# Kernel tuning notes

Measured on AMD Instinct MI355X. Metric: run time of the kernel, lower is better.

## Reference

```python
import jax, jax.numpy as jnp
import numpy as np

VOCAB, EMB_DIM = 50000, 300
HIDDEN, OUT_DIM, N_ASPECTS = 256, 3, 8
BATCH, SEQ = 8192, 128


def setup_inputs() -> dict:
    key = jax.random.key(0)
    k1, k2, k3, k4, k5, k6, k7 = jax.random.split(key, 7)
    input_ids = jax.random.randint(k1, (BATCH, SEQ), 0, VOCAB, dtype=jnp.int64 if jax.config.jax_enable_x64 else jnp.int32)
    aspect_id = jax.random.randint(k2, (BATCH,), 0, N_ASPECTS, dtype=jnp.int32)
    emb = jax.random.normal(k3, (VOCAB, EMB_DIM), dtype=jnp.float32)
    # Per-aspect 2-layer MLP params, stacked along aspect axis. PyTorch Linear
    # init scale ~ U(-1/sqrt(fan_in), 1/sqrt(fan_in)).
    s1 = 1.0 / np.sqrt(EMB_DIM)
    s2 = 1.0 / np.sqrt(HIDDEN)
    W1 = jax.random.uniform(k4, (N_ASPECTS, EMB_DIM, HIDDEN), jnp.float32, -s1, s1)
    b1 = jax.random.uniform(k5, (N_ASPECTS, HIDDEN), jnp.float32, -s1, s1)
    W2 = jax.random.uniform(k6, (N_ASPECTS, HIDDEN, OUT_DIM), jnp.float32, -s2, s2)
    b2 = jax.random.uniform(k7, (N_ASPECTS, OUT_DIM), jnp.float32, -s2, s2)
    return {"input_ids": input_ids, "aspect_id": aspect_id, "emb": emb,
            "W1": W1, "b1": b1, "W2": W2, "b2": b2}


def reference(input_ids, aspect_id, emb, W1, b1, W2, b2):
    # Embedding lookup + mean-pool over sequence -> [B, EMB_DIM]
    x = emb[input_ids].mean(axis=1)
    # Run every sample through every aspect MLP (A is tiny: 8), then select.
    # Same math as per-sample routed MLP, but as A batched GEMMs.
    h = jax.nn.relu(jnp.einsum('bd,adh->abh', x, W1) + b1[:, None, :])  # [A,B,H]
    o = jnp.einsum('abh,aho->abo', h, W2) + b2[:, None, :]              # [A,B,O]
    # Select per-sample expert output: [B, OUT_DIM]
    o_b = jnp.transpose(o, (1, 0, 2))  # [B, A, O]
    return jnp.take_along_axis(o_b, aspect_id[:, None, None], axis=1)[:, 0, :]
```

## Files before the change

### kernel.cpp

```cpp
#include <hip/hip_runtime.h>

constexpr int EMB_DIM   = 300;
constexpr int HIDDEN    = 256;
constexpr int OUT_DIM   = 3;
constexpr int SEQ       = 128;
constexpr int N_ASPECTS = 8;
constexpr int TILE      = 32;
constexpr int MTILE     = 8;

__device__ __forceinline__ unsigned int bfbits(float f) {
  unsigned int u = __float_as_uint(f);
  return (u + 0x7fffu + ((u >> 16) & 1u)) >> 16;
}
__device__ __forceinline__ unsigned int pack2(float lo, float hi) {
  return bfbits(lo) | (bfbits(hi) << 16);
}
__device__ __forceinline__ float blo(unsigned int u) { return __uint_as_float(u << 16); }
__device__ __forceinline__ float bhi(unsigned int u) { return __uint_as_float(u & 0xffff0000u); }

__global__ __launch_bounds__(1024) void prep_kernel(
    const float* __restrict__ emb, unsigned int* __restrict__ emb16, int n8,
    const float* __restrict__ W1, unsigned int* __restrict__ w16, int nw8,
    const int* __restrict__ aspect, int B, int* __restrict__ perm, int nperm) {
  const int t = threadIdx.x;

  if (blockIdx.x != 0) {
    int i = (blockIdx.x - 1) * 1024 + t;
    const int stride = (gridDim.x - 1) * 1024;
    const int total8 = n8 + nw8;
    for (; i < total8; i += stride) {
      const float4* p;
      unsigned int* dst;
      int k;
      if (i < n8) { p = (const float4*)emb + (size_t)i * 2;        dst = emb16; k = i; }
      else        { p = (const float4*)W1  + (size_t)(i - n8) * 2; dst = w16;   k = i - n8; }
      float4 a = p[0], b = p[1];
      uint4 o;
      o.x = pack2(a.x, a.y); o.y = pack2(a.z, a.w);
      o.z = pack2(b.x, b.y); o.w = pack2(b.z, b.w);
      ((uint4*)dst)[k] = o;
    }
    return;
  }

  const int lane = t & 63, wave = t >> 6;
  __shared__ int wcnt[16][N_ASPECTS];
  __shared__ int cur[16][N_ASPECTS];

  for (int i = t; i < nperm; i += 1024) perm[i] = -1;

  int my_a[8];
  int cnt[N_ASPECTS];
#pragma unroll
  for (int q = 0; q < N_ASPECTS; ++q) cnt[q] = 0;
#pragma unroll
  for (int k = 0; k < 8; ++k) {
    int s = t + k * 1024;
    int a = (s < B) ? aspect[s] : -1;
    my_a[k] = a;
#pragma unroll
    for (int q = 0; q < N_ASPECTS; ++q) cnt[q] += (a == q);
  }
#pragma unroll
  for (int q = 0; q < N_ASPECTS; ++q) {
    int c = cnt[q];
    for (int off = 32; off > 0; off >>= 1) c += __shfl_down(c, off);
    if (lane == 0) wcnt[wave][q] = c;
  }
  __syncthreads();
  if (t == 0) {
    int base = 0;
    for (int q = 0; q < N_ASPECTS; ++q) {
      int tot = 0;
      for (int w = 0; w < 16; ++w) { cur[w][q] = base + tot; tot += wcnt[w][q]; }
      base += ((tot + TILE - 1) / TILE) * TILE;
    }
  }
  __syncthreads();

#pragma unroll
  for (int k = 0; k < 8; ++k) {
    int a = my_a[k];
    int s = t + k * 1024;
#pragma unroll
    for (int q = 0; q < N_ASPECTS; ++q) {
      unsigned long long m = __ballot(a == q);
      if (a == q) {
        int rank = __popcll(m & ((1ull << lane) - 1ull));
        int pos = cur[wave][q] + rank;
        perm[pos] = s;
        if (rank == __popcll(m) - 1) cur[wave][q] = pos + 1;
      }
    }
  }
}

__global__ __launch_bounds__(256) void pool_kernel(
    const int* __restrict__ ids, const unsigned short* __restrict__ emb16,
    float* __restrict__ x, int B) {
  const int wave = threadIdx.x >> 6, lane = threadIdx.x & 63;
  const int b = blockIdx.x * 4 + wave;
  if (b >= B) return;

  int r0 = ids[(size_t)b * SEQ + lane];
  int r1 = ids[(size_t)b * SEQ + lane + 64];

#pragma unroll
  for (int k = 2; k <= 128; k <<= 1) {
#pragma unroll
    for (int j = k >> 1; j >= 1; j >>= 1) {
      if (j == 64) {
        int lo = min(r0, r1), hi = max(r0, r1);
        r0 = lo; r1 = hi;
      } else {
        const bool up0 = ((lane & k) == 0);
        const bool up1 = (((lane + 64) & k) == 0);
        const bool side = ((lane & j) == 0);
        int o0 = __shfl_xor(r0, j);
        int o1 = __shfl_xor(r1, j);
        r0 = (side == up0) ? min(r0, o0) : max(r0, o0);
        r1 = (side == up1) ? min(r1, o1) : max(r1, o1);
      }
    }
  }

  __shared__ int sid[4][SEQ];
  sid[wave][lane]      = r0;
  sid[wave][lane + 64] = r1;
  __syncthreads();

  float a0 = 0.f, a1 = 0.f, a2 = 0.f, a3 = 0.f;
  float c0 = 0.f, c1 = 0.f, c2 = 0.f, c3 = 0.f;
#pragma unroll 4
  for (int s = 0; s < SEQ; ++s) {
    const uint2* __restrict__ r =
        (const uint2*)(emb16 + (size_t)sid[wave][s] * EMB_DIM);
    uint2 v = r[lane];
    a0 += blo(v.x); a1 += bhi(v.x); a2 += blo(v.y); a3 += bhi(v.y);
    if (lane < 11) {
      uint2 w = r[64 + lane];
      c0 += blo(w.x); c1 += bhi(w.x); c2 += blo(w.y); c3 += bhi(w.y);
    }
  }
  const float sc = 1.0f / (float)SEQ;
  float4* __restrict__ xr = (float4*)(x + (size_t)b * EMB_DIM);
  xr[lane] = make_float4(a0 * sc, a1 * sc, a2 * sc, a3 * sc);
  if (lane < 11)
    xr[64 + lane] = make_float4(c0 * sc, c1 * sc, c2 * sc, c3 * sc);
}

__global__ __launch_bounds__(256) void mlp_kernel(
    const float* __restrict__ x, const int* __restrict__ aspect,
    const int* __restrict__ perm,
    const unsigned short* __restrict__ w16, const float* __restrict__ b1,
    const float* __restrict__ W2, const float* __restrict__ b2,
    float* __restrict__ out) {
  const int t = threadIdx.x;
  const int wave = t >> 6, lane = t & 63;
  const int g = wave >> 1;
  const int kw = wave & 1;
  const int start = blockIdx.x * MTILE;

  __shared__ int ss[MTILE];
  __shared__ float xch[2][4][64][4];

  if (t < MTILE) ss[t] = perm[start + t];
  __syncthreads();
  const int s0 = ss[0];
  if (s0 < 0) return;
  const int a = aspect[s0];

  int smp[4];
  const float* xrow[4];
#pragma unroll
  for (int s = 0; s < 4; ++s) {
    int m = __builtin_amdgcn_readfirstlane(ss[g * 4 + s]);
    smp[s] = m;
    xrow[s] = x + (size_t)(m < 0 ? s0 : m) * EMB_DIM;
  }

  const unsigned short* __restrict__ w1r =
      w16 + (size_t)a * EMB_DIM * HIDDEN + 4 * lane;
  float4 acc[4];
  if (kw == 0) {
    const float4 bb = ((const float4*)(b1 + a * HIDDEN))[lane];
#pragma unroll
    for (int s = 0; s < 4; ++s) acc[s] = bb;
  } else {
#pragma unroll
    for (int s = 0; s < 4; ++s) acc[s] = make_float4(0.f, 0.f, 0.f, 0.f);
  }
  const int d0 = kw ? 160 : 0;
  const int d1 = kw ? EMB_DIM : 160;
#pragma unroll 2
  for (int d = d0; d < d1; d += 4) {
    float4 xv[4];
#pragma unroll
    for (int s = 0; s < 4; ++s) xv[s] = *(const float4*)(xrow[s] + d);
#pragma unroll
    for (int dd = 0; dd < 4; ++dd) {
      const uint2 wv = *(const uint2*)(w1r + (size_t)(d + dd) * HIDDEN);
      const float w0 = blo(wv.x), w1v = bhi(wv.x);
      const float w2v = blo(wv.y), w3v = bhi(wv.y);
#pragma unroll
      for (int s = 0; s < 4; ++s) {
        const float xs = dd == 0 ? xv[s].x : dd == 1 ? xv[s].y
                        : dd == 2 ? xv[s].z : xv[s].w;
        acc[s].x = fmaf(xs, w0,  acc[s].x);
        acc[s].y = fmaf(xs, w1v, acc[s].y);
        acc[s].z = fmaf(xs, w2v, acc[s].z);
        acc[s].w = fmaf(xs, w3v, acc[s].w);
      }
    }
  }

  if (kw == 0) {
    *(float4*)&xch[g][2][lane][0] = acc[2];
    *(float4*)&xch[g][3][lane][0] = acc[3];
  } else {
    *(float4*)&xch[g][0][lane][0] = acc[0];
    *(float4*)&xch[g][1][lane][0] = acc[1];
  }
  __syncthreads();

  const float4* __restrict__ w2p =
      (const float4*)(W2 + (size_t)a * HIDDEN * OUT_DIM + lane * 12);
  const float4 w2a = w2p[0];
  const float4 w2b = w2p[1];
  const float4 w2c = w2p[2];

  float4 own[2];
  int ms[2];
  if (kw == 0) {
    own[0] = acc[0]; own[1] = acc[1];
    ms[0] = smp[0];  ms[1] = smp[1];
  } else {
    own[0] = acc[2]; own[1] = acc[3];
    ms[0] = smp[2];  ms[1] = smp[3];
  }
  const int mys = 2 * kw;

  float p[2][OUT_DIM];
#pragma unroll
  for (int i = 0; i < 2; ++i) {
    const float4 pr = *(const float4*)&xch[g][mys + i][lane][0];
    const float h0 = fmaxf(own[i].x + pr.x, 0.f);
    const float h1 = fmaxf(own[i].y + pr.y, 0.f);
    const float h2 = fmaxf(own[i].z + pr.z, 0.f);
    const float h3 = fmaxf(own[i].w + pr.w, 0.f);
    p[i][0] = fmaf(h0, w2a.x, fmaf(h1, w2a.w, fmaf(h2, w2b.z, h3 * w2c.y)));
    p[i][1] = fmaf(h0, w2a.y, fmaf(h1, w2b.x, fmaf(h2, w2b.w, h3 * w2c.z)));
    p[i][2] = fmaf(h0, w2a.z, fmaf(h1, w2b.y, fmaf(h2, w2c.x, h3 * w2c.w)));
  }
#pragma unroll
  for (int off = 32; off > 0; off >>= 1)
#pragma unroll
    for (int i = 0; i < 2; ++i) {
      p[i][0] += __shfl_down(p[i][0], off);
      p[i][1] += __shfl_down(p[i][1], off);
      p[i][2] += __shfl_down(p[i][2], off);
    }

  if (lane == 0) {
    const float g0 = b2[a * OUT_DIM + 0];
    const float g1 = b2[a * OUT_DIM + 1];
    const float g2 = b2[a * OUT_DIM + 2];
#pragma unroll
    for (int i = 0; i < 2; ++i) {
      if (ms[i] >= 0) {
        float* o = out + (size_t)ms[i] * OUT_DIM;
        o[0] = p[i][0] + g0;
        o[1] = p[i][1] + g1;
        o[2] = p[i][2] + g2;
      }
    }
  }
}

extern "C" void kernel_launch(void* const* d_in, const int* in_sizes, int n_in,
                              void* d_out, int out_size, void* d_ws, size_t ws_size,
                              hipStream_t stream) {
  const int*   ids    = (const int*)d_in[0];
  const int*   aspect = (const int*)d_in[1];
  const float* emb    = (const float*)d_in[2];
  const float* W1     = (const float*)d_in[3];
  const float* b1     = (const float*)d_in[4];
  const float* W2     = (const float*)d_in[5];
  const float* b2     = (const float*)d_in[6];
  float*       out    = (float*)d_out;

  const int B     = in_sizes[1];
  const int nemb  = in_sizes[2];
  const int nw1   = in_sizes[3];
  const int nblk  = (B + TILE - 1) / TILE + N_ASPECTS;
  const int nperm = nblk * TILE;

  float* x    = (float*)d_ws;
  int*   perm = (int*)((char*)d_ws + (size_t)B * EMB_DIM * sizeof(float));
  unsigned short* emb16 =
      (unsigned short*)((char*)perm + (((size_t)nperm * 4 + 15) & ~(size_t)15));
  unsigned short* w16 = emb16 + (size_t)nemb;

  prep_kernel<<<513, 1024, 0, stream>>>(emb, (unsigned int*)emb16, nemb / 8,
                                        W1, (unsigned int*)w16, nw1 / 8,
                                        aspect, B, perm, nperm);
  pool_kernel<<<(B + 3) / 4, 256, 0, stream>>>(ids, emb16, x, B);
  mlp_kernel<<<nperm / MTILE, 256, 0, stream>>>(x, aspect, perm, w16, b1, W2, b2, out);
}
```

Measured before the change: 129.4 us.

## Fuse embedding mean-pool into aspect-sorted MLP kernel via shared memory

Merges the pooling kernel into the MLP kernel. Each block pools its 8 aspect-sorted samples, two per wave, and keeps the pooled vectors in shared memory instead of writing x to global memory and reading it back. This removes a kernel launch and the global round trip of the pooled activations. The cost is more shared memory per block and more registers per wave. Padded perm slots now repeat pooling for sample s0, and the pooling grid follows perm order rather than batch order.

After: 120.2 us (median of 2 runs). 7.1% less time.

```diff
diff --git a/kernel.cpp b/kernel.cpp
--- a/kernel.cpp
+++ b/kernel.cpp
@@ -95,89 +95,107 @@
   }
 }
 
-__global__ __launch_bounds__(256) void pool_kernel(
+__global__ __launch_bounds__(256) void fused_kernel(
     const int* __restrict__ ids, const unsigned short* __restrict__ emb16,
-    float* __restrict__ x, int B) {
-  const int wave = threadIdx.x >> 6, lane = threadIdx.x & 63;
-  const int b = blockIdx.x * 4 + wave;
-  if (b >= B) return;
-
-  int r0 = ids[(size_t)b * SEQ + lane];
-  int r1 = ids[(size_t)b * SEQ + lane + 64];
+    const int* __restrict__ aspect, const int* __restrict__ perm,
+    const unsigned short* __restrict__ w16, const float* __restrict__ b1,
+    const float* __restrict__ W2, const float* __restrict__ b2,
+    float* __restrict__ out) {
+  const int t = threadIdx.x;
+  const int wave = t >> 6, lane = t & 63;
+  const int start = blockIdx.x * MTILE;
+
+  __shared__ int   ss[MTILE];
+  __shared__ int   sid[MTILE][SEQ];
+  __shared__ float xs[MTILE][EMB_DIM + 4];
+  __shared__ float xch[2][4][64][4];
+
+  if (t < MTILE) ss[t] = perm[start + t];
+  __syncthreads();
+  const int s0 = ss[0];
+  if (s0 < 0) return;
+  const int a = aspect[s0];
+
+  const int sa = 2 * wave, sb = 2 * wave + 1;
+  const int ma = __builtin_amdgcn_readfirstlane(ss[sa] < 0 ? s0 : ss[sa]);
+  const int mb = __builtin_amdgcn_readfirstlane(ss[sb] < 0 ? s0 : ss[sb]);
+
+  int r0 = ids[(size_t)ma * SEQ + lane];
+  int r1 = ids[(size_t)ma * SEQ + lane + 64];
+  int r2 = ids[(size_t)mb * SEQ + lane];
+  int r3 = ids[(size_t)mb * SEQ + lane + 64];
 
 #pragma unroll
   for (int k = 2; k <= 128; k <<= 1) {
 #pragma unroll
     for (int j = k >> 1; j >= 1; j >>= 1) {
       if (j == 64) {
-        int lo = min(r0, r1), hi = max(r0, r1);
-        r0 = lo; r1 = hi;
+        int lo0 = min(r0, r1), hi0 = max(r0, r1);
+        int lo1 = min(r2, r3), hi1 = max(r2, r3);
+        r0 = lo0; r1 = hi0; r2 = lo1; r3 = hi1;
       } else {
         const bool up0 = ((lane & k) == 0);
         const bool up1 = (((lane + 64) & k) == 0);
         const bool side = ((lane & j) == 0);
         int o0 = __shfl_xor(r0, j);
         int o1 = __shfl_xor(r1, j);
+        int o2 = __shfl_xor(r2, j);
+        int o3 = __shfl_xor(r3, j);
         r0 = (side == up0) ? min(r0, o0) : max(r0, o0);
         r1 = (side == up1) ? min(r1, o1) : max(r1, o1);
+        r2 = (side == up0) ? min(r2, o2) : max(r2, o2);
+        r3 = (side == up1) ? min(r3, o3) : max(r3, o3);
       }
     }
   }
 
-  __shared__ int sid[4][SEQ];
-  sid[wave][lane]      = r0;
-  sid[wave][lane + 64] = r1;
-  __syncthreads();
-
-  float a0 = 0.f, a1 = 0.f, a2 = 0.f, a3 = 0.f;
-  float c0 = 0.f, c1 = 0.f, c2 = 0.f, c3 = 0.f;
+  sid[sa][lane]      = r0;
+  sid[sa][lane + 64] = r1;
+  sid[sb][lane]      = r2;
+  sid[sb][lane + 64] = r3;
+
+  float p0 = 0.f, p1 = 0.f, p2 = 0.f, p3 = 0.f;
+  float q0 = 0.f, q1 = 0.f, q2 = 0.f, q3 = 0.f;
+  float ta0 = 0.f, ta1 = 0.f, ta2 = 0.f, ta3 = 0.f;
+  float tb0 = 0.f, tb1 = 0.f, tb2 = 0.f, tb3 = 0.f;
+  const bool tail = (lane < 11);
+
 #pragma unroll 4
   for (int s = 0; s < SEQ; ++s) {
-    const uint2* __restrict__ r =
-        (const uint2*)(emb16 + (size_t)sid[wave][s] * EMB_DIM);
-    uint2 v = r[lane];
-    a0 += blo(v.x); a1 += bhi(v.x); a2 += blo(v.y); a3 += bhi(v.y);
-    if (lane < 11) {
-      uint2 w = r[64 + lane];
-      c0 += blo(w.x); c1 += bhi(w.x); c2 += blo(w.y); c3 += bhi(w.y);
-    }
-  }
+    const uint2* __restrict__ ra =
+        (const uint2*)(emb16 + (size_t)sid[sa][s] * EMB_DIM);
+    const uint2* __restrict__ rb =
+        (const uint2*)(emb16 + (size_t)sid[sb][s] * EMB_DIM);
+    uint2 va = ra[lane];
+    uint2 vb = rb[lane];
+    p0 += blo(va.x); p1 += bhi(va.x); p2 += blo(va.y); p3 += bhi(va.y);
+    q0 += blo(vb.x); q1 += bhi(vb.x); q2 += blo(vb.y); q3 += bhi(vb.y);
+    if (tail) {
+      uint2 wa = ra[64 + lane];
+      uint2 wb = rb[64 + lane];
+      ta0 += blo(wa.x); ta1 += bhi(wa.x); ta2 += blo(wa.y); ta3 += bhi(wa.y);
+      tb0 += blo(wb.x); tb1 += bhi(wb.x); tb2 += blo(wb.y); tb3 += bhi(wb.y);
+    }
+  }
+
   const float sc = 1.0f / (float)SEQ;
-  float4* __restrict__ xr = (float4*)(x + (size_t)b * EMB_DIM);
-  xr[lane] = make_float4(a0 * sc, a1 * sc, a2 * sc, a3 * sc);
-  if (lane < 11)
-    xr[64 + lane] = make_float4(c0 * sc, c1 * sc, c2 * sc, c3 * sc);
-}
-
-__global__ __launch_bounds__(256) void mlp_kernel(
-    const float* __restrict__ x, const int* __restrict__ aspect,
-    const int* __restrict__ perm,
-    const unsigned short* __restrict__ w16, const float* __restrict__ b1,
-    const float* __restrict__ W2, const float* __restrict__ b2,
-    float* __restrict__ out) {
-  const int t = threadIdx.x;
-  const int wave = t >> 6, lane = t & 63;
+  *(float4*)&xs[sa][4 * lane] = make_float4(p0 * sc, p1 * sc, p2 * sc, p3 * sc);
+  *(float4*)&xs[sb][4 * lane] = make_float4(q0 * sc, q1 * sc, q2 * sc, q3 * sc);
+  if (tail) {
+    *(float4*)&xs[sa][256 + 4 * lane] =
+        make_float4(ta0 * sc, ta1 * sc, ta2 * sc, ta3 * sc);
+    *(float4*)&xs[sb][256 + 4 * lane] =
+        make_float4(tb0 * sc, tb1 * sc, tb2 * sc, tb3 * sc);
+  }
+  __syncthreads();
+
   const int g = wave >> 1;
   const int kw = wave & 1;
-  const int start = blockIdx.x * MTILE;
-
-  __shared__ int ss[MTILE];
-  __shared__ float xch[2][4][64][4];
-
-  if (t < MTILE) ss[t] = perm[start + t];
-  __syncthreads();
-  const int s0 = ss[0];
-  if (s0 < 0) return;
-  const int a = aspect[s0];
 
   int smp[4];
-  const float* xrow[4];
-#pragma unroll
-  for (int s = 0; s < 4; ++s) {
-    int m = __builtin_amdgcn_readfirstlane(ss[g * 4 + s]);
-    smp[s] = m;
-    xrow[s] = x + (size_t)(m < 0 ? s0 : m) * EMB_DIM;
-  }
+#pragma unroll
+  for (int s = 0; s < 4; ++s)
+    smp[s] = __builtin_amdgcn_readfirstlane(ss[g * 4 + s]);
 
   const unsigned short* __restrict__ w1r =
       w16 + (size_t)a * EMB_DIM * HIDDEN + 4 * lane;
@@ -196,7 +214,7 @@
   for (int d = d0; d < d1; d += 4) {
     float4 xv[4];
 #pragma unroll
-    for (int s = 0; s < 4; ++s) xv[s] = *(const float4*)(xrow[s] + d);
+    for (int s = 0; s < 4; ++s) xv[s] = *(const float4*)&xs[g * 4 + s][d];
 #pragma unroll
     for (int dd = 0; dd < 4; ++dd) {
       const uint2 wv = *(const uint2*)(w1r + (size_t)(d + dd) * HIDDEN);
@@ -204,12 +222,12 @@
       const float w2v = blo(wv.y), w3v = bhi(wv.y);
 #pragma unroll
       for (int s = 0; s < 4; ++s) {
-        const float xs = dd == 0 ? xv[s].x : dd == 1 ? xv[s].y
-                        : dd == 2 ? xv[s].z : xv[s].w;
-        acc[s].x = fmaf(xs, w0,  acc[s].x);
-        acc[s].y = fmaf(xs, w1v, acc[s].y);
-        acc[s].z = fmaf(xs, w2v, acc[s].z);
-        acc[s].w = fmaf(xs, w3v, acc[s].w);
+        const float xsc = dd == 0 ? xv[s].x : dd == 1 ? xv[s].y
+                         : dd == 2 ? xv[s].z : xv[s].w;
+        acc[s].x = fmaf(xsc, w0,  acc[s].x);
+        acc[s].y = fmaf(xsc, w1v, acc[s].y);
+        acc[s].z = fmaf(xsc, w2v, acc[s].z);
+        acc[s].w = fmaf(xsc, w3v, acc[s].w);
       }
     }
   }
@@ -240,7 +258,7 @@
   }
   const int mys = 2 * kw;
 
-  float p[2][OUT_DIM];
+  float pp[2][OUT_DIM];
 #pragma unroll
   for (int i = 0; i < 2; ++i) {
     const float4 pr = *(const float4*)&xch[g][mys + i][lane][0];
@@ -248,17 +266,17 @@
     const float h1 = fmaxf(own[i].y + pr.y, 0.f);
     const float h2 = fmaxf(own[i].z + pr.z, 0.f);
     const float h3 = fmaxf(own[i].w + pr.w, 0.f);
-    p[i][0] = fmaf(h0, w2a.x, fmaf(h1, w2a.w, fmaf(h2, w2b.z, h3 * w2c.y)));
-    p[i][1] = fmaf(h0, w2a.y, fmaf(h1, w2b.x, fmaf(h2, w2b.w, h3 * w2c.z)));
-    p[i][2] = fmaf(h0, w2a.z, fmaf(h1, w2b.y, fmaf(h2, w2c.x, h3 * w2c.w)));
+    pp[i][0] = fmaf(h0, w2a.x, fmaf(h1, w2a.w, fmaf(h2, w2b.z, h3 * w2c.y)));
+    pp[i][1] = fmaf(h0, w2a.y, fmaf(h1, w2b.x, fmaf(h2, w2b.w, h3 * w2c.z)));
+    pp[i][2] = fmaf(h0, w2a.z, fmaf(h1, w2b.y, fmaf(h2, w2c.x, h3 * w2c.w)));
   }
 #pragma unroll
   for (int off = 32; off > 0; off >>= 1)
 #pragma unroll
     for (int i = 0; i < 2; ++i) {
-      p[i][0] += __shfl_down(p[i][0], off);
-      p[i][1] += __shfl_down(p[i][1], off);
-      p[i][2] += __shfl_down(p[i][2], off);
+      pp[i][0] += __shfl_down(pp[i][0], off);
+      pp[i][1] += __shfl_down(pp[i][1], off);
+      pp[i][2] += __shfl_down(pp[i][2], off);
     }
 
   if (lane == 0) {
@@ -269,9 +287,9 @@
     for (int i = 0; i < 2; ++i) {
       if (ms[i] >= 0) {
         float* o = out + (size_t)ms[i] * OUT_DIM;
-        o[0] = p[i][0] + g0;
-        o[1] = p[i][1] + g1;
-        o[2] = p[i][2] + g2;
+        o[0] = pp[i][0] + g0;
+        o[1] = pp[i][1] + g1;
+        o[2] = pp[i][2] + g2;
       }
     }
   }
@@ -295,8 +313,7 @@
   const int nblk  = (B + TILE - 1) / TILE + N_ASPECTS;
   const int nperm = nblk * TILE;
 
-  float* x    = (float*)d_ws;
-  int*   perm = (int*)((char*)d_ws + (size_t)B * EMB_DIM * sizeof(float));
+  int* perm = (int*)d_ws;
   unsigned short* emb16 =
       (unsigned short*)((char*)perm + (((size_t)nperm * 4 + 15) & ~(size_t)15));
   unsigned short* w16 = emb16 + (size_t)nemb;
@@ -304,6 +321,6 @@
   prep_kernel<<<513, 1024, 0, stream>>>(emb, (unsigned int*)emb16, nemb / 8,
                                         W1, (unsigned int*)w16, nw1 / 8,
                                         aspect, B, perm, nperm);
-  pool_kernel<<<(B + 3) / 4, 256, 0, stream>>>(ids, emb16, x, B);
-  mlp_kernel<<<nperm / MTILE, 256, 0, stream>>>(x, aspect, perm, w16, b1, W2, b2, out);
-}
+  fused_kernel<<<nperm / MTILE, 256, 0, stream>>>(ids, emb16, aspect, perm,
+                                                  w16, b1, W2, b2, out);
+}
```

## Fuse embedding pooling and aspect MLP into one kernel via shared memory

Applied to the files above, without the earlier changes.

Merges the pooling and MLP kernels into a single 512-thread kernel. Each wave pools one aspect-sorted sample into shared memory, then pairs of waves compute the MLP for two samples each. This removes the pooled x round trip through global memory and one launch. In exchange, the W1 reads are amortised over 2 samples per wave instead of 4, so weight traffic from cache doubles. Pooling also now runs over padded perm slots, which duplicate sample s0.

Result: slower. 164.0 us (+26.8%).

```diff
diff --git a/kernel.cpp b/kernel.cpp
--- a/kernel.cpp
+++ b/kernel.cpp
@@ -95,15 +95,31 @@
   }
 }
 
-__global__ __launch_bounds__(256) void pool_kernel(
+__global__ __launch_bounds__(512) void fused_kernel(
     const int* __restrict__ ids, const unsigned short* __restrict__ emb16,
-    float* __restrict__ x, int B) {
-  const int wave = threadIdx.x >> 6, lane = threadIdx.x & 63;
-  const int b = blockIdx.x * 4 + wave;
-  if (b >= B) return;
-
-  int r0 = ids[(size_t)b * SEQ + lane];
-  int r1 = ids[(size_t)b * SEQ + lane + 64];
+    const int* __restrict__ aspect, const int* __restrict__ perm,
+    const unsigned short* __restrict__ w16, const float* __restrict__ b1,
+    const float* __restrict__ W2, const float* __restrict__ b2,
+    float* __restrict__ out) {
+  const int t = threadIdx.x;
+  const int wave = t >> 6, lane = t & 63;
+  const int start = blockIdx.x * MTILE;
+
+  __shared__ int   ss[MTILE];
+  __shared__ int   sid[MTILE][SEQ];
+  __shared__ float xs[MTILE][EMB_DIM + 4];
+  __shared__ float xch[4][2][64][4];
+
+  if (t < MTILE) ss[t] = perm[start + t];
+  __syncthreads();
+  const int s0 = ss[0];
+  if (s0 < 0) return;
+  const int a = aspect[s0];
+
+  const int m = __builtin_amdgcn_readfirstlane(ss[wave] < 0 ? s0 : ss[wave]);
+
+  int r0 = ids[(size_t)m * SEQ + lane];
+  int r1 = ids[(size_t)m * SEQ + lane + 64];
 
 #pragma unroll
   for (int k = 2; k <= 128; k <<= 1) {
@@ -124,102 +140,72 @@
     }
   }
 
-  __shared__ int sid[4][SEQ];
   sid[wave][lane]      = r0;
   sid[wave][lane + 64] = r1;
-  __syncthreads();
 
   float a0 = 0.f, a1 = 0.f, a2 = 0.f, a3 = 0.f;
   float c0 = 0.f, c1 = 0.f, c2 = 0.f, c3 = 0.f;
+  const bool tail = (lane < 11);
 #pragma unroll 4
   for (int s = 0; s < SEQ; ++s) {
     const uint2* __restrict__ r =
         (const uint2*)(emb16 + (size_t)sid[wave][s] * EMB_DIM);
     uint2 v = r[lane];
     a0 += blo(v.x); a1 += bhi(v.x); a2 += blo(v.y); a3 += bhi(v.y);
-    if (lane < 11) {
+    if (tail) {
       uint2 w = r[64 + lane];
       c0 += blo(w.x); c1 += bhi(w.x); c2 += blo(w.y); c3 += bhi(w.y);
     }
   }
+
   const float sc = 1.0f / (float)SEQ;
-  float4* __restrict__ xr = (float4*)(x + (size_t)b * EMB_DIM);
-  xr[lane] = make_float4(a0 * sc, a1 * sc, a2 * sc, a3 * sc);
-  if (lane < 11)
-    xr[64 + lane] = make_float4(c0 * sc, c1 * sc, c2 * sc, c3 * sc);
-}
-
-__global__ __launch_bounds__(256) void mlp_kernel(
-    const float* __restrict__ x, const int* __restrict__ aspect,
-    const int* __restrict__ perm,
-    const unsigned short* __restrict__ w16, const float* __restrict__ b1,
-    const float* __restrict__ W2, const float* __restrict__ b2,
-    float* __restrict__ out) {
-  const int t = threadIdx.x;
-  const int wave = t >> 6, lane = t & 63;
-  const int g = wave >> 1;
+  *(float4*)&xs[wave][4 * lane] = make_float4(a0 * sc, a1 * sc, a2 * sc, a3 * sc);
+  if (tail)
+    *(float4*)&xs[wave][256 + 4 * lane] =
+        make_float4(c0 * sc, c1 * sc, c2 * sc, c3 * sc);
+  __syncthreads();
+
+  const int g  = wave >> 1;
   const int kw = wave & 1;
-  const int start = blockIdx.x * MTILE;
-
-  __shared__ int ss[MTILE];
-  __shared__ float xch[2][4][64][4];
-
-  if (t < MTILE) ss[t] = perm[start + t];
-  __syncthreads();
-  const int s0 = ss[0];
-  if (s0 < 0) return;
-  const int a = aspect[s0];
-
-  int smp[4];
-  const float* xrow[4];
-#pragma unroll
-  for (int s = 0; s < 4; ++s) {
-    int m = __builtin_amdgcn_readfirstlane(ss[g * 4 + s]);
-    smp[s] = m;
-    xrow[s] = x + (size_t)(m < 0 ? s0 : m) * EMB_DIM;
-  }
 
   const unsigned short* __restrict__ w1r =
       w16 + (size_t)a * EMB_DIM * HIDDEN + 4 * lane;
-  float4 acc[4];
+  float4 acc[2];
   if (kw == 0) {
     const float4 bb = ((const float4*)(b1 + a * HIDDEN))[lane];
-#pragma unroll
-    for (int s = 0; s < 4; ++s) acc[s] = bb;
+    acc[0] = bb; acc[1] = bb;
   } else {
-#pragma unroll
-    for (int s = 0; s < 4; ++s) acc[s] = make_float4(0.f, 0.f, 0.f, 0.f);
+    acc[0] = make_float4(0.f, 0.f, 0.f, 0.f);
+    acc[1] = make_float4(0.f, 0.f, 0.f, 0.f);
   }
   const int d0 = kw ? 160 : 0;
   const int d1 = kw ? EMB_DIM : 160;
 #pragma unroll 2
   for (int d = d0; d < d1; d += 4) {
-    float4 xv[4];
-#pragma unroll
-    for (int s = 0; s < 4; ++s) xv[s] = *(const float4*)(xrow[s] + d);
+    float4 xv0 = *(const float4*)&xs[2 * g][d];
+    float4 xv1 = *(const float4*)&xs[2 * g + 1][d];
 #pragma unroll
     for (int dd = 0; dd < 4; ++dd) {
       const uint2 wv = *(const uint2*)(w1r + (size_t)(d + dd) * HIDDEN);
       const float w0 = blo(wv.x), w1v = bhi(wv.x);
       const float w2v = blo(wv.y), w3v = bhi(wv.y);
-#pragma unroll
-      for (int s = 0; s < 4; ++s) {
-        const float xs = dd == 0 ? xv[s].x : dd == 1 ? xv[s].y
-                        : dd == 2 ? xv[s].z : xv[s].w;
-        acc[s].x = fmaf(xs, w0,  acc[s].x);
-        acc[s].y = fmaf(xs, w1v, acc[s].y);
-        acc[s].z = fmaf(xs, w2v, acc[s].z);
-        acc[s].w = fmaf(xs, w3v, acc[s].w);
-      }
+      const float x0 = dd == 0 ? xv0.x : dd == 1 ? xv0.y : dd == 2 ? xv0.z : xv0.w;
+      const float x1 = dd == 0 ? xv1.x : dd == 1 ? xv1.y : dd == 2 ? xv1.z : xv1.w;
+      acc[0].x = fmaf(x0, w0,  acc[0].x);
+      acc[0].y = fmaf(x0, w1v, acc[0].y);
+      acc[0].z = fmaf(x0, w2v, acc[0].z);
+      acc[0].w = fmaf(x0, w3v, acc[0].w);
+      acc[1].x = fmaf(x1, w0,  acc[1].x);
+      acc[1].y = fmaf(x1, w1v, acc[1].y);
+      acc[1].z = fmaf(x1, w2v, acc[1].z);
+      acc[1].w = fmaf(x1, w3v, acc[1].w);
     }
   }
 
   if (kw == 0) {
-    *(float4*)&xch[g][2][lane][0] = acc[2];
-    *(float4*)&xch[g][3][lane][0] = acc[3];
+    *(float4*)&xch[g][1][lane][0] = acc[1];
   } else {
     *(float4*)&xch[g][0][lane][0] = acc[0];
-    *(float4*)&xch[g][1][lane][0] = acc[1];
   }
   __syncthreads();
 
@@ -229,51 +215,39 @@
   const float4 w2b = w2p[1];
   const float4 w2c = w2p[2];
 
-  float4 own[2];
-  int ms[2];
+  float4 own;
+  float4 pr;
+  int ms;
   if (kw == 0) {
-    own[0] = acc[0]; own[1] = acc[1];
-    ms[0] = smp[0];  ms[1] = smp[1];
+    own = acc[0];
+    pr  = *(const float4*)&xch[g][0][lane][0];
+    ms  = __builtin_amdgcn_readfirstlane(ss[2 * g]);
   } else {
-    own[0] = acc[2]; own[1] = acc[3];
-    ms[0] = smp[2];  ms[1] = smp[3];
-  }
-  const int mys = 2 * kw;
-
-  float p[2][OUT_DIM];
-#pragma unroll
-  for (int i = 0; i < 2; ++i) {
-    const float4 pr = *(const float4*)&xch[g][mys + i][lane][0];
-    const float h0 = fmaxf(own[i].x + pr.x, 0.f);
-    const float h1 = fmaxf(own[i].y + pr.y, 0.f);
-    const float h2 = fmaxf(own[i].z + pr.z, 0.f);
-    const float h3 = fmaxf(own[i].w + pr.w, 0.f);
-    p[i][0] = fmaf(h0, w2a.x, fmaf(h1, w2a.w, fmaf(h2, w2b.z, h3 * w2c.y)));
-    p[i][1] = fmaf(h0, w2a.y, fmaf(h1, w2b.x, fmaf(h2, w2b.w, h3 * w2c.z)));
-    p[i][2] = fmaf(h0, w2a.z, fmaf(h1, w2b.y, fmaf(h2, w2c.x, h3 * w2c.w)));
-  }
-#pragma unroll
-  for (int off = 32; off > 0; off >>= 1)
-#pragma unroll
-    for (int i = 0; i < 2; ++i) {
-      p[i][0] += __shfl_down(p[i][0], off);
-      p[i][1] += __shfl_down(p[i][1], off);
-      p[i][2] += __shfl_down(p[i][2], off);
-    }
-
-  if (lane == 0) {
-    const float g0 = b2[a * OUT_DIM + 0];
-    const float g1 = b2[a * OUT_DIM + 1];
-    const float g2 = b2[a * OUT_DIM + 2];
-#pragma unroll
-    for (int i = 0; i < 2; ++i) {
-      if (ms[i] >= 0) {
-        float* o = out + (size_t)ms[i] * OUT_DIM;
-        o[0] = p[i][0] + g0;
-        o[1] = p[i][1] + g1;
-        o[2] = p[i][2] + g2;
-      }
-    }
+    own = acc[1];
+    pr  = *(const float4*)&xch[g][1][lane][0];
+    ms  = __builtin_amdgcn_readfirstlane(ss[2 * g + 1]);
+  }
+
+  const float h0 = fmaxf(own.x + pr.x, 0.f);
+  const float h1 = fmaxf(own.y + pr.y, 0.f);
+  const float h2 = fmaxf(own.z + pr.z, 0.f);
+  const float h3 = fmaxf(own.w + pr.w, 0.f);
+  float p0 = fmaf(h0, w2a.x, fmaf(h1, w2a.w, fmaf(h2, w2b.z, h3 * w2c.y)));
+  float p1 = fmaf(h0, w2a.y, fmaf(h1, w2b.x, fmaf(h2, w2b.w, h3 * w2c.z)));
+  float p2 = fmaf(h0, w2a.z, fmaf(h1, w2b.y, fmaf(h2, w2c.x, h3 * w2c.w)));
+
+#pragma unroll
+  for (int off = 32; off > 0; off >>= 1) {
+    p0 += __shfl_down(p0, off);
+    p1 += __shfl_down(p1, off);
+    p2 += __shfl_down(p2, off);
+  }
+
+  if (lane == 0 && ms >= 0) {
+    float* o = out + (size_t)ms * OUT_DIM;
+    o[0] = p0 + b2[a * OUT_DIM + 0];
+    o[1] = p1 + b2[a * OUT_DIM + 1];
+    o[2] = p2 + b2[a * OUT_DIM + 2];
   }
 }
 
@@ -295,8 +269,7 @@
   const int nblk  = (B + TILE - 1) / TILE + N_ASPECTS;
   const int nperm = nblk * TILE;
 
-  float* x    = (float*)d_ws;
-  int*   perm = (int*)((char*)d_ws + (size_t)B * EMB_DIM * sizeof(float));
+  int* perm = (int*)d_ws;
   unsigned short* emb16 =
       (unsigned short*)((char*)perm + (((size_t)nperm * 4 + 15) & ~(size_t)15));
   unsigned short* w16 = emb16 + (size_t)nemb;
@@ -304,6 +277,6 @@
   prep_kernel<<<513, 1024, 0, stream>>>(emb, (unsigned int*)emb16, nemb / 8,
                                         W1, (unsigned int*)w16, nw1 / 8,
                                         aspect, B, perm, nperm);
-  pool_kernel<<<(B + 3) / 4, 256, 0, stream>>>(ids, emb16, x, B);
-  mlp_kernel<<<nperm / MTILE, 256, 0, stream>>>(x, aspect, perm, w16, b1, W2, b2, out);
-}
+  fused_kernel<<<nperm / MTILE, 512, 0, stream>>>(ids, emb16, aspect, perm,
+                                                  w16, b1, W2, b2, out);
+}
```
